# Kernel optimization log

Measured on AMD Instinct MI355X. Metric: run time of the kernel, lower is better.

The kernel has to match this reference:

```python
import jax, jax.numpy as jnp
import numpy as np

N = 100_000   # nodes per type
E = 800_000   # edges per relation
H = 128       # hidden_channels
O = 64        # out_channels
TIME_SCALE = 1.0
LN_EPS = 1e-5


def setup_inputs() -> dict:
    key = jax.random.key(0)
    ks = jax.random.split(key, 24)
    nrm = lambda k, shp, s=1.0: jax.random.normal(k, shp, jnp.float32) * s
    inp = {}
    inp["x_A"] = nrm(ks[0], (N, H))
    inp["x_B"] = nrm(ks[1], (N, H))
    inp["x_C"] = nrm(ks[2], (N, H))
    inp["t_A"] = jax.random.uniform(ks[3], (N,), jnp.float32) * 1000.0
    inp["t_B"] = jax.random.uniform(ks[4], (N,), jnp.float32) * 1000.0
    inp["t_C"] = jax.random.uniform(ks[5], (N,), jnp.float32) * 1000.0
    inp["edge1"] = jnp.stack([jax.random.randint(ks[6], (E,), 0, N),
                              jax.random.randint(ks[7], (E,), 0, N)]).astype(jnp.int32)
    inp["edge2"] = jnp.stack([jax.random.randint(ks[8], (E,), 0, N),
                              jax.random.randint(ks[9], (E,), 0, N)]).astype(jnp.int32)
    kk = 10
    for i in range(2):
        inp[f"Wl{i}"] = nrm(ks[kk], (H, H), 0.05); kk += 1
        inp[f"bl{i}"] = jnp.zeros((H,), jnp.float32)
        inp[f"W0{i}"] = nrm(ks[kk], (H, H), 0.05); kk += 1
        inp[f"b0{i}"] = jnp.zeros((H,), jnp.float32)
        inp[f"W1{i}"] = nrm(ks[kk], (H, H), 0.05); kk += 1
        inp[f"b1{i}"] = jnp.zeros((H,), jnp.float32)
        inp[f"gate{i}"] = jnp.asarray(0.5, jnp.float32)
        inp[f"lam{i}"] = jnp.asarray(0.1, jnp.float32)  # raw lambda
        inp[f"lng{i}"] = jnp.ones((H,), jnp.float32)
        inp[f"lnb{i}"] = jnp.zeros((H,), jnp.float32)
    inp["Wout"] = nrm(ks[kk], (H, O), 0.05)
    inp["bout"] = jnp.zeros((O,), jnp.float32)
    return inp


def _layer(h_src, h_dst, x0_dst, edge, t_src, t_dst,
           Wl, bl, W0, b0, W1, b1, gate, raw_lam, lng, lnb):
    s, d = edge[0], edge[1]
    n_dst = h_dst.shape[0]
    # per-edge time-decay weight
    lam = jax.nn.softplus(raw_lam) + 1e-8
    delta = jnp.maximum((t_dst[d] - t_src[s]) / TIME_SCALE, 0.0)
    w = jnp.exp(jnp.maximum(-lam * delta, -60.0))          # [E]
    # gather + weight + scatter-add  (propagate with aggr='add')
    msg = h_src[s] * w[:, None]                            # [E,H]
    agg = jax.ops.segment_sum(msg, d, num_segments=n_dst)  # [n_dst,H]
    deg = jnp.maximum(jax.ops.segment_sum(w, d, num_segments=n_dst), 1e-6)
    out = agg / deg[:, None]
    g = jax.nn.sigmoid(gate)
    y = out @ Wl + bl + (1.0 - g) * (h_dst @ W0 + b0) + g * (x0_dst @ W1 + b1)
    y = jax.nn.relu(y)
    mu = jnp.mean(y, axis=-1, keepdims=True)
    var = jnp.mean((y - mu) ** 2, axis=-1, keepdims=True)
    y = (y - mu) * jax.lax.rsqrt(var + LN_EPS) * lng + lnb
    # index_copy_: only nodes that appear as a destination get updated
    cnt = jax.ops.segment_sum(jnp.ones_like(w), d, num_segments=n_dst)
    return jnp.where((cnt > 0)[:, None], y, h_dst)


def reference(x_A, x_B, x_C, t_A, t_B, t_C, edge1, edge2,
              Wl0, bl0, W00, b00, W10, b10, gate0, lam0, lng0, lnb0,
              Wl1, bl1, W01, b01, W11, b11, gate1, lam1, lng1, lnb1,
              Wout, bout):
    # reversed(metapath): process (B,r2,C) with conv_idx=1 first, then (A,r1,B) with conv_idx=0
    h_C = _layer(x_B, x_C, x_C, edge2, t_B, t_C,
                 Wl1, bl1, W01, b01, W11, b11, gate1, lam1, lng1, lnb1)
    h_B = _layer(x_A, x_B, x_B, edge1, t_A, t_B,
                 Wl0, bl0, W00, b00, W10, b10, gate0, lam0, lng0, lnb0)
    del h_B  # target type is metapath[-1][2] == 'C'; B's update does not feed C
    return h_C @ Wout + bout
```

## Files before the change

### kernel.cpp

```cpp
#include <hip/hip_runtime.h>


#define HD 128
#define OD 64
#define SCAN_E 1024

typedef unsigned short u16;
typedef short v8s __attribute__((ext_vector_type(8)));
typedef float v4f __attribute__((ext_vector_type(4)));

union Frag {
    unsigned int u[4];
    uint4 q;
    v8s v;
};

__device__ __forceinline__ float softplus_f(float x) {
    return fmaxf(x, 0.0f) + log1pf(expf(-fabsf(x)));
}
__device__ __forceinline__ float sigmoid_f(float x) {
    return 1.0f / (1.0f + expf(-x));
}

__device__ __forceinline__ void split_store(float x, u16* ph, u16* pl) {
    unsigned int b = __float_as_uint(x);
    unsigned int h = b & 0xffff0000u;
    *ph = (u16)(h >> 16);
    float r = x - __uint_as_float(h);
    *pl = (u16)(__float_as_uint(r) >> 16);
}

__device__ __forceinline__ void cvt_split8(const float* f, unsigned int* hi,
                                           unsigned int* lo) {
#pragma unroll
    for (int j = 0; j < 4; ++j) {
        unsigned int b0 = __float_as_uint(f[2 * j]);
        unsigned int b1 = __float_as_uint(f[2 * j + 1]);
        unsigned int h0 = b0 & 0xffff0000u;
        unsigned int h1 = b1 & 0xffff0000u;
        hi[j] = (h0 >> 16) | h1;
        float r0 = f[2 * j]     - __uint_as_float(h0);
        float r1 = f[2 * j + 1] - __uint_as_float(h1);
        lo[j] = (__float_as_uint(r0) >> 16) | (__float_as_uint(r1) & 0xffff0000u);
    }
}

__global__ __launch_bounds__(256) void k_hist(
    const int* __restrict__ edge, int* __restrict__ cnt, int E)
{
    int e = blockIdx.x * 256 + threadIdx.x;
    if (e < E) atomicAdd(cnt + edge[E + e], 1);
}

__global__ __launch_bounds__(256) void k_scan1(
    const int* __restrict__ cnt, int* __restrict__ offs,
    int* __restrict__ part, int N)
{
    __shared__ int sh[256];
    const int t = threadIdx.x;
    const int base = blockIdx.x * SCAN_E + t * 4;
    int v[4], sum = 0;
#pragma unroll
    for (int i = 0; i < 4; ++i) {
        int idx = base + i;
        v[i] = (idx < N) ? cnt[idx] : 0;
        sum += v[i];
    }
    sh[t] = sum;
    __syncthreads();
    for (int off = 1; off < 256; off <<= 1) {
        int x = (t >= off) ? sh[t - off] : 0;
        __syncthreads();
        sh[t] += x;
        __syncthreads();
    }
    int run = (t > 0) ? sh[t - 1] : 0;
    if (t == 255) part[blockIdx.x] = sh[t];
#pragma unroll
    for (int i = 0; i < 4; ++i) {
        int idx = base + i;
        if (idx < N) offs[idx] = run;
        run += v[i];
    }
}

__global__ __launch_bounds__(128) void k_scan2(int* __restrict__ part, int NB)
{
    __shared__ int sh[128];
    const int t = threadIdx.x;
    sh[t] = (t < NB) ? part[t] : 0;
    __syncthreads();
    for (int off = 1; off < 128; off <<= 1) {
        int x = (t >= off) ? sh[t - off] : 0;
        __syncthreads();
        sh[t] += x;
        __syncthreads();
    }
    if (t < NB) part[t] = (t > 0) ? sh[t - 1] : 0;
}

__global__ __launch_bounds__(256) void k_fillw(
    const int* __restrict__ edge, const float* __restrict__ tB,
    const float* __restrict__ tC, const float* __restrict__ lam_raw,
    const int* __restrict__ offs, const int* __restrict__ part,
    int* __restrict__ fillc, int2* __restrict__ srcw, int E)
{
    int e = blockIdx.x * 256 + threadIdx.x;
    if (e >= E) return;
    int s = edge[e];
    int d = edge[E + e];
    float lam = softplus_f(lam_raw[0]) + 1e-8f;
    float dt  = fmaxf(tC[d] - tB[s], 0.0f);
    float w   = expf(fmaxf(-lam * dt, -60.0f));
    int pos = offs[d] + part[d >> 10] + atomicAdd(fillc + d, 1);
    srcw[pos] = make_int2(s, __float_as_int(w));
}

__global__ __launch_bounds__(256) void k_wprep(
    const float* __restrict__ Wl, const float* __restrict__ W0,
    const float* __restrict__ W1, const float* __restrict__ Wout,
    const float* __restrict__ bl, const float* __restrict__ b0,
    const float* __restrict__ b1, const float* __restrict__ gatep,
    u16* __restrict__ wlh, u16* __restrict__ wll,
    u16* __restrict__ wch, u16* __restrict__ wcl,
    u16* __restrict__ woh, u16* __restrict__ wol, float* __restrict__ bc)
{
    int i = blockIdx.x * 256 + threadIdx.x;
    const float g = sigmoid_f(gatep[0]);
    if (i < 16384) {
        int n = i >> 7, k = i & 127;
        float a  = Wl[k * 128 + n];
        float w0 = W0[k * 128 + n];
        float w1 = W1[k * 128 + n];
        float c  = (1.f - g) * w0 + g * w1;
        int off = ((k >> 5) * 128 + n) * 32 + (k & 31);
        split_store(a, wlh + off, wll + off);
        split_store(c, wch + off, wcl + off);
    } else if (i < 24576) {
        int j = i - 16384;
        int n = j >> 7, k = j & 127;
        float v = Wout[k * 64 + n];
        int off = ((k >> 5) * 64 + n) * 32 + (k & 31);
        split_store(v, woh + off, wol + off);
    } else if (i < 24704) {
        int t = i - 24576;
        bc[t] = bl[t] + (1.f - g) * b0[t] + g * b1[t];
    }
}

__global__ __launch_bounds__(256) void k_gather(
    const float* __restrict__ xB, const int2* __restrict__ srcw,
    const int* __restrict__ offs, const int* __restrict__ part,
    const int* __restrict__ cnt, float* __restrict__ aggn, int N)
{
    const int wave = (blockIdx.x * 256 + threadIdx.x) >> 6;
    const int lane = threadIdx.x & 63;
    const int half = lane >> 5;
    const int l5   = lane & 31;
    if (wave >= N) return;
    const int r    = wave;
    const int degc = cnt[r];

    float4* dst = reinterpret_cast<float4*>(aggn + (size_t)r * HD) + l5;
    if (degc == 0) {
        if (half == 0) *dst = make_float4(0.f, 0.f, 0.f, 0.f);
        return;
    }

    const int start = offs[r] + part[r >> 10];
    float4 acc = make_float4(0.f, 0.f, 0.f, 0.f);
    float sumw = 0.f;
#pragma unroll 2
    for (int j = half; j < degc; j += 2) {
        int2 sw = srcw[start + j];
        float w = __int_as_float(sw.y);
        const float4 x = *(reinterpret_cast<const float4*>(
                               xB + (size_t)sw.x * HD) + l5);
        acc.x = fmaf(w, x.x, acc.x);
        acc.y = fmaf(w, x.y, acc.y);
        acc.z = fmaf(w, x.z, acc.z);
        acc.w = fmaf(w, x.w, acc.w);
        sumw += w;
    }
    acc.x += __shfl_xor(acc.x, 32);
    acc.y += __shfl_xor(acc.y, 32);
    acc.z += __shfl_xor(acc.z, 32);
    acc.w += __shfl_xor(acc.w, 32);
    sumw  += __shfl_xor(sumw, 32);
    float inv = 1.0f / fmaxf(sumw, 1e-6f);
    if (half == 0) {
        acc.x *= inv; acc.y *= inv; acc.z *= inv; acc.w *= inv;
        *dst = acc;
    }
}

__global__ __launch_bounds__(256) void k_layer_mfma(
    const float* __restrict__ xC, float* __restrict__ buf,
    const int* __restrict__ cnt,
    const u16* __restrict__ wlh, const u16* __restrict__ wll,
    const u16* __restrict__ wch, const u16* __restrict__ wcl,
    const float* __restrict__ bc, const float* __restrict__ lng,
    const float* __restrict__ lnb, int N)
{
    const int lane = threadIdx.x & 63;
    const int wid  = threadIdx.x >> 6;
    const int lr   = lane & 15;
    const int kb   = lane >> 4;
    const int row0 = blockIdx.x * 128 + wid * 32;

    v4f acc[2][8] = {};

#pragma unroll
    for (int mat = 0; mat < 2; ++mat) {
        const float* Asrc = mat ? xC : buf;
        const uint4* BH = (const uint4*)(mat ? wch : wlh);
        const uint4* BL = (const uint4*)(mat ? wcl : wll);
#pragma unroll
        for (int kc = 0; kc < 4; ++kc) {
            Frag ah[2], al[2];
#pragma unroll
            for (int rt = 0; rt < 2; ++rt) {
                int r = row0 + rt * 16 + lr;
                r = (r < N) ? r : (N - 1);
                const float4* ap = (const float4*)(
                    Asrc + (size_t)r * HD + kc * 32 + kb * 8);
                float4 u0 = ap[0], u1 = ap[1];
                float f[8] = {u0.x, u0.y, u0.z, u0.w, u1.x, u1.y, u1.z, u1.w};
                cvt_split8(f, ah[rt].u, al[rt].u);
            }
#pragma unroll
            for (int ct = 0; ct < 8; ++ct) {
                int idx = kc * 512 + (ct * 16 + lr) * 4 + kb;
                Frag bh, bl;
                bh.q = BH[idx];
                bl.q = BL[idx];
#pragma unroll
                for (int rt = 0; rt < 2; ++rt) {
                    acc[rt][ct] = __builtin_amdgcn_mfma_f32_16x16x32_bf16(
                        ah[rt].v, bh.v, acc[rt][ct], 0, 0, 0);
                    acc[rt][ct] = __builtin_amdgcn_mfma_f32_16x16x32_bf16(
                        ah[rt].v, bl.v, acc[rt][ct], 0, 0, 0);
                    acc[rt][ct] = __builtin_amdgcn_mfma_f32_16x16x32_bf16(
                        al[rt].v, bh.v, acc[rt][ct], 0, 0, 0);
                }
            }
        }
    }

    float bcv[8], gav[8], bev[8];
#pragma unroll
    for (int ct = 0; ct < 8; ++ct) {
        int c = ct * 16 + lr;
        bcv[ct] = bc[c];
        gav[ct] = lng[c];
        bev[ct] = lnb[c];
    }

#pragma unroll
    for (int rt = 0; rt < 2; ++rt) {
        int rq = row0 + rt * 16 + kb * 4;
        int cvr[4] = {0, 0, 0, 0};
        if (rq < N) {
            int4 cv = *(const int4*)(cnt + rq);
            cvr[0] = cv.x; cvr[1] = cv.y; cvr[2] = cv.z; cvr[3] = cv.w;
        }
#pragma unroll
        for (int reg = 0; reg < 4; ++reg) {
            float yv[8];
            float s = 0.f, q = 0.f;
#pragma unroll
            for (int ct = 0; ct < 8; ++ct) {
                float v = acc[rt][ct][reg] + bcv[ct];
                v = fmaxf(v, 0.0f);
                yv[ct] = v;
                s += v;
                q += v * v;
            }
#pragma unroll
            for (int m = 1; m < 16; m <<= 1) {
                s += __shfl_xor(s, m);
                q += __shfl_xor(q, m);
            }
            float mu   = s * (1.0f / 128.0f);
            float var  = q * (1.0f / 128.0f) - mu * mu;
            float rstd = rsqrtf(var + 1e-5f);

            int r = rq + reg;
            if (r < N) {
                size_t base = (size_t)r * HD;
                if (cvr[reg] > 0) {
#pragma unroll
                    for (int ct = 0; ct < 8; ++ct)
                        buf[base + ct * 16 + lr] =
                            (yv[ct] - mu) * rstd * gav[ct] + bev[ct];
                } else {
#pragma unroll
                    for (int ct = 0; ct < 8; ++ct)
                        buf[base + ct * 16 + lr] = xC[base + ct * 16 + lr];
                }
            }
        }
    }
}

__global__ __launch_bounds__(256) void k_out_mfma(
    const float* __restrict__ hC, const u16* __restrict__ woh,
    const u16* __restrict__ wol, const float* __restrict__ bout,
    float* __restrict__ out, int N)
{
    const int lane = threadIdx.x & 63;
    const int wid  = threadIdx.x >> 6;
    const int lr   = lane & 15;
    const int kb   = lane >> 4;
    const int row0 = blockIdx.x * 128 + wid * 32;

    v4f acc[2][4] = {};
    const uint4* BH = (const uint4*)woh;
    const uint4* BL = (const uint4*)wol;

#pragma unroll
    for (int kc = 0; kc < 4; ++kc) {
        Frag ah[2], al[2];
#pragma unroll
        for (int rt = 0; rt < 2; ++rt) {
            int r = row0 + rt * 16 + lr;
            r = (r < N) ? r : (N - 1);
            const float4* ap = (const float4*)(
                hC + (size_t)r * HD + kc * 32 + kb * 8);
            float4 u0 = ap[0], u1 = ap[1];
            float f[8] = {u0.x, u0.y, u0.z, u0.w, u1.x, u1.y, u1.z, u1.w};
            cvt_split8(f, ah[rt].u, al[rt].u);
        }
#pragma unroll
        for (int ct = 0; ct < 4; ++ct) {
            int idx = kc * 256 + (ct * 16 + lr) * 4 + kb;
            Frag bh, bl;
            bh.q = BH[idx];
            bl.q = BL[idx];
#pragma unroll
            for (int rt = 0; rt < 2; ++rt) {
                acc[rt][ct] = __builtin_amdgcn_mfma_f32_16x16x32_bf16(
                    ah[rt].v, bh.v, acc[rt][ct], 0, 0, 0);
                acc[rt][ct] = __builtin_amdgcn_mfma_f32_16x16x32_bf16(
                    ah[rt].v, bl.v, acc[rt][ct], 0, 0, 0);
                acc[rt][ct] = __builtin_amdgcn_mfma_f32_16x16x32_bf16(
                    al[rt].v, bh.v, acc[rt][ct], 0, 0, 0);
            }
        }
    }

    float bov[4];
#pragma unroll
    for (int ct = 0; ct < 4; ++ct) bov[ct] = bout[ct * 16 + lr];

#pragma unroll
    for (int rt = 0; rt < 2; ++rt) {
#pragma unroll
        for (int reg = 0; reg < 4; ++reg) {
            int r = row0 + rt * 16 + kb * 4 + reg;
            if (r < N) {
#pragma unroll
                for (int ct = 0; ct < 4; ++ct)
                    out[(size_t)r * OD + ct * 16 + lr] =
                        acc[rt][ct][reg] + bov[ct];
            }
        }
    }
}

extern "C" void kernel_launch(void* const* d_in, const int* in_sizes, int n_in,
                              void* d_out, int out_size, void* d_ws, size_t ws_size,
                              hipStream_t stream) {
    const float* xB    = (const float*)d_in[1];
    const float* xC    = (const float*)d_in[2];
    const float* tB    = (const float*)d_in[4];
    const float* tC    = (const float*)d_in[5];
    const int*   edge2 = (const int*)d_in[7];
    const float* Wl1   = (const float*)d_in[18];
    const float* bl1   = (const float*)d_in[19];
    const float* W01   = (const float*)d_in[20];
    const float* b01   = (const float*)d_in[21];
    const float* W11   = (const float*)d_in[22];
    const float* b11   = (const float*)d_in[23];
    const float* gate1 = (const float*)d_in[24];
    const float* lam1  = (const float*)d_in[25];
    const float* lng1  = (const float*)d_in[26];
    const float* lnb1  = (const float*)d_in[27];
    const float* Wout  = (const float*)d_in[28];
    const float* bout  = (const float*)d_in[29];

    const int N = in_sizes[2] / HD;
    const int E = in_sizes[7] / 2;

    int*   cnt   = (int*)d_ws;
    int*   fillc = cnt + N;
    int*   offs  = fillc + N;
    int*   part  = offs + N;
    int2*  srcw  = (int2*)(part + 128);
    u16*   wlh   = (u16*)(srcw + E);
    u16*   wll   = wlh + 16384;
    u16*   wch   = wll + 16384;
    u16*   wcl   = wch + 16384;
    u16*   woh   = wcl + 16384;
    u16*   wol   = woh + 8192;
    float* bc    = (float*)(wol + 8192);
    float* buf   = bc + 128;

    hipMemsetAsync(cnt, 0, (size_t)2 * N * sizeof(int), stream);

    dim3 blk(256);
    const int gE = (E + 255) / 256;
    const int NB = (N + SCAN_E - 1) / SCAN_E;

    k_wprep<<<97, blk, 0, stream>>>(Wl1, W01, W11, Wout, bl1, b01, b11, gate1,
                                    wlh, wll, wch, wcl, woh, wol, bc);
    k_hist <<<gE, blk, 0, stream>>>(edge2, cnt, E);
    k_scan1<<<NB, blk, 0, stream>>>(cnt, offs, part, N);
    k_scan2<<<1, 128, 0, stream>>>(part, NB);
    k_fillw<<<gE, blk, 0, stream>>>(edge2, tB, tC, lam1, offs, part, fillc, srcw, E);

    const int gN64 = (N * 64 + 255) / 256;
    k_gather<<<gN64, blk, 0, stream>>>(xB, srcw, offs, part, cnt, buf, N);

    const int GB = (N + 127) / 128;
    k_layer_mfma<<<GB, blk, 0, stream>>>(xC, buf, cnt, wlh, wll, wch, wcl,
                                         bc, lng1, lnb1, N);
    k_out_mfma  <<<GB, blk, 0, stream>>>(buf, woh, wol, bout, (float*)d_out, N);
}
```

Before: 237.0 us.

## Fuse layer GEMM+LayerNorm with output projection via swizzled LDS; widen gather lanes

The layer MFMA kernel and the output-projection kernel become one kernel. The normalized hidden tile now sits in XOR-swizzled shared memory instead of a round trip through a global buffer, which removes one kernel launch and a 100k×128 float write plus re-read. The gather kernel now processes four edges at a time per wave, with 16 lanes each loading two float4s per row instead of two edges with 32 lanes, which adds memory-level parallelism. The fused kernel uses 64KB of LDS per block, which may reduce occupancy.

```diff
diff --git a/kernel.cpp b/kernel.cpp
--- a/kernel.cpp
+++ b/kernel.cpp
@@ -20,6 +20,10 @@
 }
 __device__ __forceinline__ float sigmoid_f(float x) {
     return 1.0f / (1.0f + expf(-x));
+}
+__device__ __forceinline__ int swz(int r, int c) {
+    int g = (c >> 2) ^ (r & 7);
+    return r * 128 + g * 4 + (c & 3);
 }
 
 __device__ __forceinline__ void split_store(float x, u16* ph, u16* pl) {
@@ -155,64 +159,77 @@
 {
     const int wave = (blockIdx.x * 256 + threadIdx.x) >> 6;
     const int lane = threadIdx.x & 63;
-    const int half = lane >> 5;
-    const int l5   = lane & 31;
+    const int slot = lane >> 4;
+    const int l4   = lane & 15;
     if (wave >= N) return;
     const int r    = wave;
     const int degc = cnt[r];
 
-    float4* dst = reinterpret_cast<float4*>(aggn + (size_t)r * HD) + l5;
+    float* dstp = aggn + (size_t)r * HD;
     if (degc == 0) {
-        if (half == 0) *dst = make_float4(0.f, 0.f, 0.f, 0.f);
+        if (slot == 0) {
+            *reinterpret_cast<float4*>(dstp + l4 * 4) = make_float4(0, 0, 0, 0);
+            *reinterpret_cast<float4*>(dstp + 64 + l4 * 4) = make_float4(0, 0, 0, 0);
+        }
         return;
     }
 
     const int start = offs[r] + part[r >> 10];
-    float4 acc = make_float4(0.f, 0.f, 0.f, 0.f);
-    float sumw = 0.f;
-#pragma unroll 2
-    for (int j = half; j < degc; j += 2) {
-        int2 sw = srcw[start + j];
-        float w = __int_as_float(sw.y);
-        const float4 x = *(reinterpret_cast<const float4*>(
-                               xB + (size_t)sw.x * HD) + l5);
-        acc.x = fmaf(w, x.x, acc.x);
-        acc.y = fmaf(w, x.y, acc.y);
-        acc.z = fmaf(w, x.z, acc.z);
-        acc.w = fmaf(w, x.w, acc.w);
-        sumw += w;
-    }
-    acc.x += __shfl_xor(acc.x, 32);
-    acc.y += __shfl_xor(acc.y, 32);
-    acc.z += __shfl_xor(acc.z, 32);
-    acc.w += __shfl_xor(acc.w, 32);
-    sumw  += __shfl_xor(sumw, 32);
-    float inv = 1.0f / fmaxf(sumw, 1e-6f);
-    if (half == 0) {
-        acc.x *= inv; acc.y *= inv; acc.z *= inv; acc.w *= inv;
-        *dst = acc;
-    }
-}
-
-__global__ __launch_bounds__(256) void k_layer_mfma(
-    const float* __restrict__ xC, float* __restrict__ buf,
+    float4 a0 = make_float4(0, 0, 0, 0), a1 = make_float4(0, 0, 0, 0);
+    float sw = 0.f;
+    for (int j = slot; j < degc; j += 4) {
+        int2 swp = srcw[start + j];
+        float w = __int_as_float(swp.y);
+        const float* row = xB + (size_t)swp.x * HD;
+        float4 x0 = *reinterpret_cast<const float4*>(row + l4 * 4);
+        float4 x1 = *reinterpret_cast<const float4*>(row + 64 + l4 * 4);
+        a0.x = fmaf(w, x0.x, a0.x); a0.y = fmaf(w, x0.y, a0.y);
+        a0.z = fmaf(w, x0.z, a0.z); a0.w = fmaf(w, x0.w, a0.w);
+        a1.x = fmaf(w, x1.x, a1.x); a1.y = fmaf(w, x1.y, a1.y);
+        a1.z = fmaf(w, x1.z, a1.z); a1.w = fmaf(w, x1.w, a1.w);
+        sw += w;
+    }
+#pragma unroll
+    for (int m = 16; m <= 32; m <<= 1) {
+        a0.x += __shfl_xor(a0.x, m); a0.y += __shfl_xor(a0.y, m);
+        a0.z += __shfl_xor(a0.z, m); a0.w += __shfl_xor(a0.w, m);
+        a1.x += __shfl_xor(a1.x, m); a1.y += __shfl_xor(a1.y, m);
+        a1.z += __shfl_xor(a1.z, m); a1.w += __shfl_xor(a1.w, m);
+        sw   += __shfl_xor(sw, m);
+    }
+    float inv = 1.0f / fmaxf(sw, 1e-6f);
+    if (slot == 0) {
+        a0.x *= inv; a0.y *= inv; a0.z *= inv; a0.w *= inv;
+        a1.x *= inv; a1.y *= inv; a1.z *= inv; a1.w *= inv;
+        *reinterpret_cast<float4*>(dstp + l4 * 4) = a0;
+        *reinterpret_cast<float4*>(dstp + 64 + l4 * 4) = a1;
+    }
+}
+
+__global__ __launch_bounds__(256) void k_fused(
+    const float* __restrict__ xC, const float* __restrict__ aggn,
     const int* __restrict__ cnt,
     const u16* __restrict__ wlh, const u16* __restrict__ wll,
     const u16* __restrict__ wch, const u16* __restrict__ wcl,
+    const u16* __restrict__ woh, const u16* __restrict__ wol,
     const float* __restrict__ bc, const float* __restrict__ lng,
-    const float* __restrict__ lnb, int N)
-{
+    const float* __restrict__ lnb, const float* __restrict__ bout,
+    float* __restrict__ out, int N)
+{
+    __shared__ float lds[4 * 32 * 128];
+
     const int lane = threadIdx.x & 63;
     const int wid  = threadIdx.x >> 6;
     const int lr   = lane & 15;
     const int kb   = lane >> 4;
     const int row0 = blockIdx.x * 128 + wid * 32;
+    float* myl = lds + wid * 32 * 128;
 
     v4f acc[2][8] = {};
 
 #pragma unroll
     for (int mat = 0; mat < 2; ++mat) {
-        const float* Asrc = mat ? xC : buf;
+        const float* Asrc = mat ? xC : aggn;
         const uint4* BH = (const uint4*)(mat ? wch : wlh);
         const uint4* BL = (const uint4*)(mat ? wcl : wll);
 #pragma unroll
@@ -266,6 +283,8 @@
         }
 #pragma unroll
         for (int reg = 0; reg < 4; ++reg) {
+            int rloc = rt * 16 + kb * 4 + reg;
+            int r    = rq + reg;
             float yv[8];
             float s = 0.f, q = 0.f;
 #pragma unroll
@@ -285,36 +304,29 @@
             float var  = q * (1.0f / 128.0f) - mu * mu;
             float rstd = rsqrtf(var + 1e-5f);
 
-            int r = rq + reg;
             if (r < N) {
-                size_t base = (size_t)r * HD;
                 if (cvr[reg] > 0) {
 #pragma unroll
                     for (int ct = 0; ct < 8; ++ct)
-                        buf[base + ct * 16 + lr] =
+                        myl[swz(rloc, ct * 16 + lr)] =
                             (yv[ct] - mu) * rstd * gav[ct] + bev[ct];
                 } else {
+                    size_t base = (size_t)r * HD;
 #pragma unroll
                     for (int ct = 0; ct < 8; ++ct)
-                        buf[base + ct * 16 + lr] = xC[base + ct * 16 + lr];
+                        myl[swz(rloc, ct * 16 + lr)] = xC[base + ct * 16 + lr];
                 }
-            }
-        }
-    }
-}
-
-__global__ __launch_bounds__(256) void k_out_mfma(
-    const float* __restrict__ hC, const u16* __restrict__ woh,
-    const u16* __restrict__ wol, const float* __restrict__ bout,
-    float* __restrict__ out, int N)
-{
-    const int lane = threadIdx.x & 63;
-    const int wid  = threadIdx.x >> 6;
-    const int lr   = lane & 15;
-    const int kb   = lane >> 4;
-    const int row0 = blockIdx.x * 128 + wid * 32;
-
-    v4f acc[2][4] = {};
+            } else {
+#pragma unroll
+                for (int ct = 0; ct < 8; ++ct)
+                    myl[swz(rloc, ct * 16 + lr)] = 0.0f;
+            }
+        }
+    }
+
+    __syncthreads();
+
+    v4f acc2[2][4] = {};
     const uint4* BH = (const uint4*)woh;
     const uint4* BL = (const uint4*)wol;
 
@@ -323,11 +335,10 @@
         Frag ah[2], al[2];
 #pragma unroll
         for (int rt = 0; rt < 2; ++rt) {
-            int r = row0 + rt * 16 + lr;
-            r = (r < N) ? r : (N - 1);
-            const float4* ap = (const float4*)(
-                hC + (size_t)r * HD + kc * 32 + kb * 8);
-            float4 u0 = ap[0], u1 = ap[1];
+            int rloc = rt * 16 + lr;
+            int c0   = kc * 32 + kb * 8;
+            float4 u0 = *reinterpret_cast<const float4*>(&myl[swz(rloc, c0)]);
+            float4 u1 = *reinterpret_cast<const float4*>(&myl[swz(rloc, c0 + 4)]);
             float f[8] = {u0.x, u0.y, u0.z, u0.w, u1.x, u1.y, u1.z, u1.w};
             cvt_split8(f, ah[rt].u, al[rt].u);
         }
@@ -339,12 +350,12 @@
             bl.q = BL[idx];
 #pragma unroll
             for (int rt = 0; rt < 2; ++rt) {
-                acc[rt][ct] = __builtin_amdgcn_mfma_f32_16x16x32_bf16(
-                    ah[rt].v, bh.v, acc[rt][ct], 0, 0, 0);
-                acc[rt][ct] = __builtin_amdgcn_mfma_f32_16x16x32_bf16(
-                    ah[rt].v, bl.v, acc[rt][ct], 0, 0, 0);
-                acc[rt][ct] = __builtin_amdgcn_mfma_f32_16x16x32_bf16(
-                    al[rt].v, bh.v, acc[rt][ct], 0, 0, 0);
+                acc2[rt][ct] = __builtin_amdgcn_mfma_f32_16x16x32_bf16(
+                    ah[rt].v, bh.v, acc2[rt][ct], 0, 0, 0);
+                acc2[rt][ct] = __builtin_amdgcn_mfma_f32_16x16x32_bf16(
+                    ah[rt].v, bl.v, acc2[rt][ct], 0, 0, 0);
+                acc2[rt][ct] = __builtin_amdgcn_mfma_f32_16x16x32_bf16(
+                    al[rt].v, bh.v, acc2[rt][ct], 0, 0, 0);
             }
         }
     }
@@ -362,7 +373,7 @@
 #pragma unroll
                 for (int ct = 0; ct < 4; ++ct)
                     out[(size_t)r * OD + ct * 16 + lr] =
-                        acc[rt][ct][reg] + bov[ct];
+                        acc2[rt][ct][reg] + bov[ct];
             }
         }
     }
@@ -423,7 +434,6 @@
     k_gather<<<gN64, blk, 0, stream>>>(xB, srcw, offs, part, cnt, buf, N);
 
     const int GB = (N + 127) / 128;
-    k_layer_mfma<<<GB, blk, 0, stream>>>(xC, buf, cnt, wlh, wll, wch, wcl,
-                                         bc, lng1, lnb1, N);
-    k_out_mfma  <<<GB, blk, 0, stream>>>(buf, woh, wol, bout, (float*)d_out, N);
-}
+    k_fused<<<GB, blk, 0, stream>>>(xC, buf, cnt, wlh, wll, wch, wcl, woh, wol,
+                                    bc, lng1, lnb1, bout, (float*)d_out, N);
+}
```

After: 220.4 us. -7.0%, faster.
